# Optimization experiments

Measured on AMD Instinct MI355X. Metric: run time of the kernel, lower is better.

The kernel has to match this reference:

```python
import jax, jax.numpy as jnp
import numpy as np

N_NODES = 50000
N_EDGES = 400000


def setup_inputs() -> dict:
    key = jax.random.key(0)
    k1, k2, k3, k4 = jax.random.split(key, 4)
    in_feat = jax.random.normal(k1, (2, 64, 4, N_NODES), dtype=jnp.float32)
    src = jax.random.randint(k2, (N_EDGES,), 0, N_NODES, dtype=jnp.int32)
    dst = jax.random.randint(k3, (N_EDGES,), 0, N_NODES, dtype=jnp.int32)
    W = jax.random.normal(k4, (64, 64), dtype=jnp.float32) * (1.0 / 8.0)
    b = jnp.zeros((64,), dtype=jnp.float32)
    return {"in_feat": in_feat, "src": src, "dst": dst, "W": W, "b": b}


def reference(in_feat, src, dst, W, b):
    # in_feat: (B, h, T, N). Net permutation [3,1,2,0] then [0,3,2,1] == [3,0,2,1]
    x = jnp.transpose(in_feat, (3, 0, 2, 1))  # (N, B, T, h) -- node-major for GraphConv
    N = x.shape[0]
    ones_e = jnp.ones(src.shape[0], dtype=x.dtype)
    deg_out = jnp.clip(jax.ops.segment_sum(ones_e, src, num_segments=N), 1.0)
    deg_in = jnp.clip(jax.ops.segment_sum(ones_e, dst, num_segments=N), 1.0)
    # DGL GraphConv, norm='both', in_feats == out_feats -> aggregate then matmul
    x = x * jax.lax.rsqrt(deg_out)[:, None, None, None]
    agg = jax.ops.segment_sum(x[src], dst, num_segments=N)  # (N, B, T, h)
    agg = agg * jax.lax.rsqrt(deg_in)[:, None, None, None]
    h = jnp.einsum('nbth,hf->nbtf', agg, W) + b
    h = jax.nn.relu(h)
    # inverse permutation [0,3,2,1] then [3,1,2,0] == transpose(h, (1,3,2,0))
    out = jnp.transpose(h, (1, 3, 2, 0))  # (B, h, T, N)
    return jax.nn.relu(out)
```

## Files before the change

### kernel.cpp

```cpp
#include <hip/hip_runtime.h>
#include <hip/hip_fp16.h>


typedef _Float16 half8 __attribute__((ext_vector_type(8)));
typedef float f32x4 __attribute__((ext_vector_type(4)));

extern "C" __global__ void k_deg(const int* __restrict__ src, const int* __restrict__ dst,
                                 int* __restrict__ deg_out, int* __restrict__ deg_in, int E) {
  int e = blockIdx.x * blockDim.x + threadIdx.x;
  if (e < E) {
    atomicAdd(&deg_out[src[e]], 1);
    atomicAdd(&deg_in[dst[e]], 1);
  }
}

extern "C" __global__ __launch_bounds__(256) void k_scan1(const int* __restrict__ deg_in,
                                                          const int* __restrict__ deg_out,
                                                          int* __restrict__ bsum,
                                                          float* __restrict__ rs_out,
                                                          float* __restrict__ rs_in, int N) {
  __shared__ int red[256];
  int tid = threadIdx.x;
  int i = blockIdx.x * 256 + tid;
  int di = (i < N) ? deg_in[i] : 0;
  red[tid] = di;
  if (i < N) {
    int a = deg_out[i] > 1 ? deg_out[i] : 1;
    int b = di > 1 ? di : 1;
    rs_out[i] = rsqrtf((float)a);
    rs_in[i]  = rsqrtf((float)b);
  }
  __syncthreads();
  #pragma unroll
  for (int off = 128; off > 0; off >>= 1) {
    if (tid < off) red[tid] += red[tid + off];
    __syncthreads();
  }
  if (tid == 0) bsum[blockIdx.x] = red[0];
}

extern "C" __global__ __launch_bounds__(256) void k_scan3(const int* __restrict__ deg,
                                                          const int* __restrict__ bsum,
                                                          int* __restrict__ offs,
                                                          int* __restrict__ cursor,
                                                          int M, int N) {
  __shared__ int sc[256];
  __shared__ int bs[256];
  int tid = threadIdx.x;

  int bv = (tid < M) ? bsum[tid] : 0;
  bs[tid] = bv;
  __syncthreads();
  #pragma unroll
  for (int off = 1; off < 256; off <<= 1) {
    int t = bs[tid];
    if (tid >= off) t += bs[tid - off];
    __syncthreads();
    bs[tid] = t;
    __syncthreads();
  }
  int boff = (blockIdx.x > 0) ? bs[blockIdx.x - 1] : 0;
  if (blockIdx.x == 0 && tid == 0) offs[N] = bs[255];

  int i = blockIdx.x * 256 + tid;
  int v = (i < N) ? deg[i] : 0;
  sc[tid] = v;
  __syncthreads();
  #pragma unroll
  for (int off = 1; off < 256; off <<= 1) {
    int t = sc[tid];
    if (tid >= off) t += sc[tid - off];
    __syncthreads();
    sc[tid] = t;
    __syncthreads();
  }
  if (i < N) {
    int o = boff + sc[tid] - v;
    offs[i] = o;
    cursor[i] = o;
  }
}

extern "C" __global__ void k_scatter(const int* __restrict__ src, const int* __restrict__ dst,
                                     int* __restrict__ cursor,
                                     int* __restrict__ csr_src, int E) {
  int e = blockIdx.x * blockDim.x + threadIdx.x;
  if (e < E) {
    int pos = atomicAdd(&cursor[dst[e]], 1);
    csr_src[pos] = src[e];
  }
}

extern "C" __global__ __launch_bounds__(256) void k_transform(
    const float* __restrict__ in_feat, const float* __restrict__ W,
    const float* __restrict__ rs_out, __half* __restrict__ y, int N) {
  __shared__ __half xs[64][68];
  __shared__ __half yt[64][72];
  int tid = threadIdx.x;
  int wave = tid >> 6, l = tid & 63;
  int col = l & 15;
  int kg  = l >> 4;
  int n0 = blockIdx.x * 64;

  half8 wf[4][2];
  #pragma unroll
  for (int ft = 0; ft < 4; ++ft)
    #pragma unroll
    for (int ks = 0; ks < 2; ++ks)
      #pragma unroll
      for (int j = 0; j < 8; ++j)
        wf[ft][ks][j] = (_Float16)W[(ks * 32 + kg * 8 + j) * 64 + ft * 16 + col];

  int hq = tid >> 4, nq = tid & 15;
  int nb = n0 + 4 * nq;
  float rs4[4];
  #pragma unroll
  for (int c = 0; c < 4; ++c)
    rs4[c] = (nb + c < N) ? rs_out[nb + c] : 0.0f;
  bool full4 = (nb + 3 < N);

  #pragma unroll
  for (int p = 0; p < 2; ++p) {
    int bt = blockIdx.y * 2 + p;
    int b = bt >> 2, t = bt & 3;
    const float* xbase = in_feat + (size_t)(b * 256 + t) * (size_t)N;

    __syncthreads();
    #pragma unroll
    for (int i = 0; i < 4; ++i) {
      int h = hq + 16 * i;
      const float* xp = xbase + (size_t)h * 4 * (size_t)N + nb;
      float v0 = 0.f, v1 = 0.f, v2 = 0.f, v3 = 0.f;
      if (full4) {
        float4 v = *(const float4*)xp;
        v0 = v.x; v1 = v.y; v2 = v.z; v3 = v.w;
      } else {
        if (nb < N)     v0 = xp[0];
        if (nb + 1 < N) v1 = xp[1];
        if (nb + 2 < N) v2 = xp[2];
      }
      __half2 h0 = __float22half2_rn(make_float2(v0 * rs4[0], v1 * rs4[1]));
      __half2 h1 = __float22half2_rn(make_float2(v2 * rs4[2], v3 * rs4[3]));
      uint2 u;
      u.x = *(unsigned int*)&h0;
      u.y = *(unsigned int*)&h1;
      *(uint2*)&xs[h][4 * nq] = u;
    }
    __syncthreads();

    int nloc = 16 * wave + col;
    half8 a0, a1;
    #pragma unroll
    for (int j = 0; j < 8; ++j) a0[j] = (_Float16)xs[kg * 8 + j][nloc];
    #pragma unroll
    for (int j = 0; j < 8; ++j) a1[j] = (_Float16)xs[32 + kg * 8 + j][nloc];

    #pragma unroll
    for (int ft = 0; ft < 4; ++ft) {
      f32x4 acc = {0.f, 0.f, 0.f, 0.f};
      acc = __builtin_amdgcn_mfma_f32_16x16x32_f16(a0, wf[ft][0], acc, 0, 0, 0);
      acc = __builtin_amdgcn_mfma_f32_16x16x32_f16(a1, wf[ft][1], acc, 0, 0, 0);
      #pragma unroll
      for (int r = 0; r < 4; ++r)
        yt[16 * wave + kg * 4 + r][ft * 16 + col] = __float2half(acc[r]);
    }
    __syncthreads();

    int node = tid >> 2, sg = tid & 3;
    int nr = n0 + node;
    if (nr < N) {
      uint4* gp = (uint4*)(y + (size_t)nr * 512 + bt * 64);
      gp[sg]     = *(const uint4*)&yt[node][sg * 8];
      gp[sg + 4] = *(const uint4*)&yt[node][(sg + 4) * 8];
    }
  }
}

extern "C" __global__ __launch_bounds__(512) void k_aggregate(
    const __half* __restrict__ y, const int* __restrict__ offs,
    const int* __restrict__ csr_src, const float* __restrict__ rs_in,
    const float* __restrict__ bvec, float* __restrict__ out, int N) {
  __shared__ float agg[16 * 513];
  int tid = threadIdx.x;
  int lane = tid & 63, wave = tid >> 6;
  int n0 = blockIdx.x * 16;

#define ACC_EDGE(s)                                                          \
  {                                                                          \
    const uint2* rp = (const uint2*)(y + (size_t)(s) * 512);                 \
    uint2 ua = rp[lane];                                                     \
    uint2 ub = rp[64 + lane];                                                \
    float2 f;                                                                \
    f = __half22float2(*(const __half2*)&ua.x); accA.x += f.x; accA.y += f.y;\
    f = __half22float2(*(const __half2*)&ua.y); accA.z += f.x; accA.w += f.y;\
    f = __half22float2(*(const __half2*)&ub.x); accB.x += f.x; accB.y += f.y;\
    f = __half22float2(*(const __half2*)&ub.y); accB.z += f.x; accB.w += f.y;\
  }

  #pragma unroll
  for (int k = 0; k < 2; ++k) {
    int nl = k * 8 + wave;
    int n = n0 + nl;
    float4 accA = {0.f, 0.f, 0.f, 0.f};
    float4 accB = {0.f, 0.f, 0.f, 0.f};
    if (n < N) {
      int j0 = offs[n], j1 = offs[n + 1];
      for (int base = j0; base < j1; base += 64) {
        int idxv = csr_src[base + lane];
        int m = j1 - base; if (m > 64) m = 64;
        int e = 0;
        for (; e + 3 < m; e += 4) {
          int s0 = __builtin_amdgcn_readlane(idxv, e);
          int s1 = __builtin_amdgcn_readlane(idxv, e + 1);
          int s2 = __builtin_amdgcn_readlane(idxv, e + 2);
          int s3 = __builtin_amdgcn_readlane(idxv, e + 3);
          ACC_EDGE(s0); ACC_EDGE(s1); ACC_EDGE(s2); ACC_EDGE(s3);
        }
        for (; e < m; ++e) {
          int s0 = __builtin_amdgcn_readlane(idxv, e);
          ACC_EDGE(s0);
        }
      }
    }
    *(float4*)&agg[nl * 513 + lane * 4] = accA;
    *(float4*)&agg[nl * 513 + 256 + lane * 4] = accB;
  }
#undef ACC_EDGE
  __syncthreads();

  int nl = tid & 15;
  int r0 = tid >> 4;
  int n = n0 + nl;
  float rs = (n < N) ? rs_in[n] : 0.0f;
  #pragma unroll 4
  for (int it = 0; it < 16; ++it) {
    int c = it * 32 + r0;
    float v = agg[nl * 513 + c];
    int f = c & 63, bt = c >> 6;
    int b = bt >> 2, t = bt & 3;
    v = v * rs + bvec[f];
    v = fmaxf(v, 0.0f);
    if (n < N)
      __builtin_nontemporal_store(v, &out[(size_t)((b * 64 + f) * 4 + t) * (size_t)N + n]);
  }
}

extern "C" void kernel_launch(void* const* d_in, const int* in_sizes, int n_in,
                              void* d_out, int out_size, void* d_ws, size_t ws_size,
                              hipStream_t stream) {
  const float* in_feat = (const float*)d_in[0];
  const int*   src     = (const int*)d_in[1];
  const int*   dst     = (const int*)d_in[2];
  const float* W       = (const float*)d_in[3];
  const float* bvec    = (const float*)d_in[4];
  float* out = (float*)d_out;

  int N = in_sizes[0] / 512;
  int E = in_sizes[1];

  int A  = (N + 64) & ~63;
  int EA = (E + 63) & ~63;
  int M  = (N + 255) / 256;
  int GX = (N + 63) / 64;

  int*   deg_out_i = (int*)d_ws;
  int*   deg_in_i  = deg_out_i + A;
  int*   cursor    = deg_in_i + A;
  int*   offs      = cursor + A;
  int*   bsum      = offs + A;
  float* rs_out    = (float*)(bsum + 256);
  float* rs_in     = rs_out + A;
  int*   csr_src   = (int*)(rs_in + A);
  __half* y        = (__half*)(csr_src + EA);

  hipMemsetAsync(deg_out_i, 0, (size_t)(2 * A) * sizeof(int), stream);
  hipLaunchKernelGGL(k_deg, dim3((E + 255) / 256), dim3(256), 0, stream,
                     src, dst, deg_out_i, deg_in_i, E);
  hipLaunchKernelGGL(k_scan1, dim3(M), dim3(256), 0, stream,
                     deg_in_i, deg_out_i, bsum, rs_out, rs_in, N);
  hipLaunchKernelGGL(k_scan3, dim3(M), dim3(256), 0, stream,
                     deg_in_i, bsum, offs, cursor, M, N);
  hipLaunchKernelGGL(k_scatter, dim3((E + 255) / 256), dim3(256), 0, stream,
                     src, dst, cursor, csr_src, E);
  hipLaunchKernelGGL(k_transform, dim3(GX, 4), dim3(256), 0, stream,
                     in_feat, W, rs_out, y, N);
  hipLaunchKernelGGL(k_aggregate, dim3((N + 15) / 16), dim3(512), 0, stream,
                     y, offs, csr_src, rs_in, bvec, out, N);
}
```

Measured before the change: 173.6 us.

## Move W matmul from transform kernel into aggregate epilogue after gather

Result: slower. 179.5 us (+3.4%).

```diff
diff --git a/kernel.cpp b/kernel.cpp
--- a/kernel.cpp
+++ b/kernel.cpp
@@ -91,25 +91,21 @@
   }
 }
 
-extern "C" __global__ __launch_bounds__(256) void k_transform(
-    const float* __restrict__ in_feat, const float* __restrict__ W,
-    const float* __restrict__ rs_out, __half* __restrict__ y, int N) {
+extern "C" __global__ __launch_bounds__(256) void k_wt(const float* __restrict__ W,
+                                                       __half* __restrict__ Wt) {
+  int tid = threadIdx.x;
+  for (int i = tid; i < 4096; i += 256) {
+    int f = i >> 6, h = i & 63;
+    Wt[f * 64 + h] = __float2half(W[h * 64 + f]);
+  }
+}
+
+extern "C" __global__ __launch_bounds__(256) void k_convert(
+    const float* __restrict__ in_feat, const float* __restrict__ rs_out,
+    __half* __restrict__ xh, int N) {
   __shared__ __half xs[64][68];
-  __shared__ __half yt[64][72];
-  int tid = threadIdx.x;
-  int wave = tid >> 6, l = tid & 63;
-  int col = l & 15;
-  int kg  = l >> 4;
+  int tid = threadIdx.x;
   int n0 = blockIdx.x * 64;
-
-  half8 wf[4][2];
-  #pragma unroll
-  for (int ft = 0; ft < 4; ++ft)
-    #pragma unroll
-    for (int ks = 0; ks < 2; ++ks)
-      #pragma unroll
-      for (int j = 0; j < 8; ++j)
-        wf[ft][ks][j] = (_Float16)W[(ks * 32 + kg * 8 + j) * 64 + ft * 16 + col];
 
   int hq = tid >> 4, nq = tid & 15;
   int nb = n0 + 4 * nq;
@@ -118,6 +114,9 @@
   for (int c = 0; c < 4; ++c)
     rs4[c] = (nb + c < N) ? rs_out[nb + c] : 0.0f;
   bool full4 = (nb + 3 < N);
+
+  int node = tid >> 2, sg = tid & 3;
+  int nr = n0 + node;
 
   #pragma unroll
   for (int p = 0; p < 2; ++p) {
@@ -148,30 +147,13 @@
     }
     __syncthreads();
 
-    int nloc = 16 * wave + col;
-    half8 a0, a1;
-    #pragma unroll
-    for (int j = 0; j < 8; ++j) a0[j] = (_Float16)xs[kg * 8 + j][nloc];
-    #pragma unroll
-    for (int j = 0; j < 8; ++j) a1[j] = (_Float16)xs[32 + kg * 8 + j][nloc];
-
-    #pragma unroll
-    for (int ft = 0; ft < 4; ++ft) {
-      f32x4 acc = {0.f, 0.f, 0.f, 0.f};
-      acc = __builtin_amdgcn_mfma_f32_16x16x32_f16(a0, wf[ft][0], acc, 0, 0, 0);
-      acc = __builtin_amdgcn_mfma_f32_16x16x32_f16(a1, wf[ft][1], acc, 0, 0, 0);
+    if (nr < N) {
+      __half tmp[16];
       #pragma unroll
-      for (int r = 0; r < 4; ++r)
-        yt[16 * wave + kg * 4 + r][ft * 16 + col] = __float2half(acc[r]);
-    }
-    __syncthreads();
-
-    int node = tid >> 2, sg = tid & 3;
-    int nr = n0 + node;
-    if (nr < N) {
-      uint4* gp = (uint4*)(y + (size_t)nr * 512 + bt * 64);
-      gp[sg]     = *(const uint4*)&yt[node][sg * 8];
-      gp[sg + 4] = *(const uint4*)&yt[node][(sg + 4) * 8];
+      for (int u = 0; u < 16; ++u) tmp[u] = xs[sg * 16 + u][node];
+      uint4* gp = (uint4*)(xh + (size_t)nr * 512 + bt * 64 + sg * 16);
+      gp[0] = *(const uint4*)&tmp[0];
+      gp[1] = *(const uint4*)&tmp[8];
     }
   }
 }
@@ -179,6 +161,7 @@
 extern "C" __global__ __launch_bounds__(512) void k_aggregate(
     const __half* __restrict__ y, const int* __restrict__ offs,
     const int* __restrict__ csr_src, const float* __restrict__ rs_in,
+    const __half* __restrict__ Wt,
     const float* __restrict__ bvec, float* __restrict__ out, int N) {
   __shared__ float agg[16 * 513];
   int tid = threadIdx.x;
@@ -228,20 +211,37 @@
 #undef ACC_EDGE
   __syncthreads();
 
-  int nl = tid & 15;
-  int r0 = tid >> 4;
-  int n = n0 + nl;
-  float rs = (n < N) ? rs_in[n] : 0.0f;
-  #pragma unroll 4
-  for (int it = 0; it < 16; ++it) {
-    int c = it * 32 + r0;
-    float v = agg[nl * 513 + c];
-    int f = c & 63, bt = c >> 6;
-    int b = bt >> 2, t = bt & 3;
-    v = v * rs + bvec[f];
-    v = fmaxf(v, 0.0f);
-    if (n < N)
-      __builtin_nontemporal_store(v, &out[(size_t)((b * 64 + f) * 4 + t) * (size_t)N + n]);
+  int bt = wave;
+  int b = bt >> 2, t = bt & 3;
+  int col = lane & 15, kg = lane >> 4;
+  int n = n0 + col;
+  float rsi = (n < N) ? rs_in[n] : 0.0f;
+
+  half8 xb0, xb1;
+  #pragma unroll
+  for (int j = 0; j < 8; ++j)
+    xb0[j] = (_Float16)(agg[col * 513 + bt * 64 + kg * 8 + j] * rsi);
+  #pragma unroll
+  for (int j = 0; j < 8; ++j)
+    xb1[j] = (_Float16)(agg[col * 513 + bt * 64 + 32 + kg * 8 + j] * rsi);
+
+  #pragma unroll
+  for (int ft = 0; ft < 4; ++ft) {
+    uint4 w0u = *(const uint4*)(Wt + ((ft * 16 + col) * 64 + kg * 8));
+    uint4 w1u = *(const uint4*)(Wt + ((ft * 16 + col) * 64 + 32 + kg * 8));
+    half8 w0 = *(const half8*)&w0u;
+    half8 w1 = *(const half8*)&w1u;
+    f32x4 acc = {0.f, 0.f, 0.f, 0.f};
+    acc = __builtin_amdgcn_mfma_f32_16x16x32_f16(w0, xb0, acc, 0, 0, 0);
+    acc = __builtin_amdgcn_mfma_f32_16x16x32_f16(w1, xb1, acc, 0, 0, 0);
+    #pragma unroll
+    for (int r = 0; r < 4; ++r) {
+      int f = ft * 16 + kg * 4 + r;
+      float v = acc[r] + bvec[f];
+      v = fmaxf(v, 0.0f);
+      if (n < N)
+        __builtin_nontemporal_store(v, &out[(size_t)((b * 64 + f) * 4 + t) * (size_t)N + n]);
+    }
   }
 }
 
@@ -263,15 +263,16 @@
   int M  = (N + 255) / 256;
   int GX = (N + 63) / 64;
 
-  int*   deg_out_i = (int*)d_ws;
-  int*   deg_in_i  = deg_out_i + A;
-  int*   cursor    = deg_in_i + A;
-  int*   offs      = cursor + A;
-  int*   bsum      = offs + A;
-  float* rs_out    = (float*)(bsum + 256);
-  float* rs_in     = rs_out + A;
-  int*   csr_src   = (int*)(rs_in + A);
-  __half* y        = (__half*)(csr_src + EA);
+  int*    deg_out_i = (int*)d_ws;
+  int*    deg_in_i  = deg_out_i + A;
+  int*    cursor    = deg_in_i + A;
+  int*    offs      = cursor + A;
+  int*    bsum      = offs + A;
+  __half* Wt        = (__half*)(bsum + 256);
+  float*  rs_out    = (float*)(Wt + 4096);
+  float*  rs_in     = rs_out + A;
+  int*    csr_src   = (int*)(rs_in + A);
+  __half* xh        = (__half*)(csr_src + EA);
 
   hipMemsetAsync(deg_out_i, 0, (size_t)(2 * A) * sizeof(int), stream);
   hipLaunchKernelGGL(k_deg, dim3((E + 255) / 256), dim3(256), 0, stream,
@@ -282,8 +283,9 @@
                      deg_in_i, bsum, offs, cursor, M, N);
   hipLaunchKernelGGL(k_scatter, dim3((E + 255) / 256), dim3(256), 0, stream,
                      src, dst, cursor, csr_src, E);
-  hipLaunchKernelGGL(k_transform, dim3(GX, 4), dim3(256), 0, stream,
-                     in_feat, W, rs_out, y, N);
+  hipLaunchKernelGGL(k_wt, dim3(1), dim3(256), 0, stream, W, Wt);
+  hipLaunchKernelGGL(k_convert, dim3(GX, 4), dim3(256), 0, stream,
+                     in_feat, rs_out, xh, N);
   hipLaunchKernelGGL(k_aggregate, dim3((N + 15) / 16), dim3(512), 0, stream,
-                     y, offs, csr_src, rs_in, bvec, out, N);
-}
+                     xh, offs, csr_src, rs_in, Wt, bvec, out, N);
+}
```
